# Kernel tuning notes

Measured on AMD Instinct MI355X. Metric: run time of the kernel, lower is better.

Reference implementation:

```python
import jax, jax.numpy as jnp
import numpy as np
from jax import lax

B, S, H = 32, 512, 128
NEG_INF = -1e30  # matches util.masked_softmax's large negative fill


def setup_inputs() -> dict:
    key = jax.random.key(0)
    ks = jax.random.split(key, 10)
    sc = 0.05
    vp = jax.random.normal(ks[0], (B, S, 2 * H), dtype=jnp.float32)
    # valid lengths in [S//2, S]; packed loop runs max(lengths) steps
    p_s_lengths = jax.random.randint(ks[1], (B,), S // 2, S + 1, dtype=jnp.int32)
    W_vP  = jax.random.normal(ks[2], (H, 2 * H), dtype=jnp.float32) * sc      # linear_vP.weight
    W_vPt = jax.random.normal(ks[3], (H, 2 * H), dtype=jnp.float32) * sc      # linear_vPt.weight
    w_vT  = jax.random.normal(ks[4], (H,), dtype=jnp.float32) * sc            # linear_vT.weight (1,H) -> vector
    W_g   = jax.random.normal(ks[5], (4 * H, 4 * H), dtype=jnp.float32) * sc  # g.weight
    W_ih  = jax.random.normal(ks[6], (3 * H, 4 * H), dtype=jnp.float32) * sc  # GRUCell.weight_ih
    W_hh  = jax.random.normal(ks[7], (3 * H, H), dtype=jnp.float32) * sc      # GRUCell.weight_hh
    b_ih  = jax.random.normal(ks[8], (3 * H,), dtype=jnp.float32) * sc
    b_hh  = jax.random.normal(ks[9], (3 * H,), dtype=jnp.float32) * sc
    return dict(vp=vp, p_s_lengths=p_s_lengths, W_vP=W_vP, W_vPt=W_vPt,
                w_vT=w_vT, W_g=W_g, W_ih=W_ih, W_hh=W_hh, b_ih=b_ih, b_hh=b_hh)


def _self_attn_rnn(vp, p_s_lengths, W_vP, W_vPt, w_vT, W_g, W_ih, W_hh, b_ih, b_hh):
    Bb, Ss, H2 = vp.shape
    Hh = H2 // 2
    s_idx = jnp.arange(Ss)

    # reverse_enc: reverse each sequence only over its valid prefix
    rev_idx = jnp.where(s_idx[None, :] < p_s_lengths[:, None],
                        p_s_lengths[:, None] - 1 - s_idx[None, :], s_idx[None, :])
    rev_vp = jnp.take_along_axis(vp, rev_idx[:, :, None], axis=1)

    bidir_vp = jnp.concatenate([vp, rev_vp], axis=0)       # (2B,S,2H) inputs per step
    vp2 = jnp.concatenate([vp, vp], axis=0)                 # (2B,S,2H) attention memory (forward order!)
    len2 = jnp.concatenate([p_s_lengths, p_s_lengths], 0)   # (2B,)

    keyp = jnp.einsum('bsd,hd->bsh', vp2, W_vP)             # precompute linear_vP(vp)
    seq_mask = s_idx[None, :] < len2[:, None]               # (2B,S)

    def step(h, inputs):
        x_t, active = inputs                                # (2B,2H), (2B,)
        q = x_t @ W_vPt.T                                   # (2B,H)
        logits = jnp.tanh(keyp + q[:, None, :]) @ w_vT      # (2B,S)
        a = jax.nn.softmax(jnp.where(seq_mask, logits, NEG_INF), axis=1)
        ct = jnp.einsum('bs,bsd->bd', a, vp2)               # (2B,2H)
        vpc = jnp.concatenate([x_t, ct], axis=-1)           # (2B,4H)
        gt = jax.nn.sigmoid(vpc @ W_g.T)
        xin = gt * vpc
        gi = xin @ W_ih.T + b_ih
        gh = h @ W_hh.T + b_hh
        ir, iz, inn = jnp.split(gi, 3, axis=-1)
        hr, hz, hn = jnp.split(gh, 3, axis=-1)
        r = jax.nn.sigmoid(ir + hr)
        z = jax.nn.sigmoid(iz + hz)
        n = jnp.tanh(inn + r * hn)
        h_new = (1.0 - z) * n + z * h
        # packed semantics: inactive (padded) slots keep zeros and never update again
        h_new = jnp.where(active[:, None], h_new, 0.0)
        return h_new, h_new

    xs = (jnp.swapaxes(bidir_vp, 0, 1), seq_mask.T)          # (S,2B,2H), (S,2B)
    h0 = jnp.zeros((2 * Bb, Hh), dtype=vp.dtype)
    _, hs = lax.scan(jax.checkpoint(step), h0, xs)           # hs: (S,2B,H)
    hp = jnp.swapaxes(hs, 0, 1)                              # (2B,S,H)
    # original concatenates fwd half and rev half on feature dim (rev half stays in reversed time order)
    return jnp.concatenate([hp[:Bb], hp[Bb:]], axis=-1)      # (B,S,2H)


def reference(vp, p_s_lengths, W_vP, W_vPt, w_vT, W_g, W_ih, W_hh, b_ih, b_hh):
    # dropout is identity at inference (training=False)
    return _self_attn_rnn(vp, p_s_lengths, W_vP, W_vPt, w_vT, W_g, W_ih, W_hh, b_ih, b_hh)
```

## Files before the change

kernel.cpp:

```cpp
#include <hip/hip_runtime.h>
#include <hip/hip_fp16.h>

#define BB 32
#define SS 512
#define HH 128
#define D2 256
#define D3 384
#define D4 512

#define OFF_TK  0
#define OFF_TQ  (OFF_TK + BB*SS*HH)
#define OFF_CT  (OFF_TQ + BB*SS*HH)
#define OFF_GI  (OFF_CT + BB*SS*D2)
#define OFF_F16 (OFF_GI + BB*SS*D3)
#define F16_WG  0
#define F16_WIH (F16_WG + D4*D4)
#define F16_W2  (F16_WIH + D3*D4)

typedef _Float16 f16x8 __attribute__((ext_vector_type(8)));
typedef _Float16 f16x4 __attribute__((ext_vector_type(4)));
typedef float    f32x4 __attribute__((ext_vector_type(4)));
typedef _Float16 h2_t  __attribute__((ext_vector_type(2)));

__device__ __forceinline__ float fast_tanh(float x) {
  float ax = fabsf(x);
  float e  = __expf(-2.0f * ax);
  float t  = __fdividef(1.0f - e, 1.0f + e);
  return x < 0.0f ? -t : t;
}
__device__ __forceinline__ float sigm(float x) {
  return __fdividef(1.0f, 1.0f + __expf(-x));
}

__global__ __launch_bounds__(256) void k0_prep(
    const float* __restrict__ Wg, const float* __restrict__ Wih,
    const float* __restrict__ Wvp, const float* __restrict__ Wvpt,
    float* __restrict__ ws) {
  int i = blockIdx.x * 256 + threadIdx.x;
  _Float16* f16b = (_Float16*)(ws + OFF_F16);
  if (i < D4 * D4) {
    f16b[F16_WG + i] = (_Float16)Wg[i];
  } else if (i < D4 * D4 + D3 * D4) {
    int j = i - D4 * D4;
    f16b[F16_WIH + j] = (_Float16)Wih[j];
  } else {
    int j = i - D4 * D4 - D3 * D4;
    f16b[F16_W2 + j] = (_Float16)(j < HH * D2 ? Wvp[j] : Wvpt[j - HH * D2]);
  }
}

__global__ __launch_bounds__(256, 2) void k1_keyq(const float* __restrict__ vp,
                                                  float* __restrict__ ws) {
  __shared__ __align__(16) _Float16 vpH[64 * 256];
  int tid = threadIdx.x;
  int rows0 = blockIdx.x * 64;

  #pragma unroll
  for (int i = 0; i < 8; ++i) {
    int u = tid + i * 256;
    int r = u >> 5, c8 = u & 31;
    const float* src = vp + (size_t)(rows0 + r) * D2 + c8 * 8;
    float4 a = *(const float4*)src;
    float4 b = *(const float4*)(src + 4);
    f16x8 h;
    h[0]=(_Float16)a.x; h[1]=(_Float16)a.y; h[2]=(_Float16)a.z; h[3]=(_Float16)a.w;
    h[4]=(_Float16)b.x; h[5]=(_Float16)b.y; h[6]=(_Float16)b.z; h[7]=(_Float16)b.w;
    *(f16x8*)(&vpH[r * 256 + (c8 ^ (r & 7)) * 8]) = h;
  }
  __syncthreads();

  const _Float16* W2 = (const _Float16*)(ws + OFF_F16) + F16_W2;
  int w = tid >> 6, l = tid & 63;
  int lr = l & 15, lk = (l >> 4) * 8;

  f32x4 acc[4][4];
  #pragma unroll
  for (int m = 0; m < 4; ++m)
    #pragma unroll
    for (int n = 0; n < 4; ++n) acc[m][n] = (f32x4){0.f, 0.f, 0.f, 0.f};

  for (int kc = 0; kc < 8; ++kc) {
    int k = kc * 32 + lk;
    f16x8 bf[4];
    #pragma unroll
    for (int n = 0; n < 4; ++n) {
      int r = n * 16 + lr;
      bf[n] = *(const f16x8*)(&vpH[r * 256 + (((k >> 3) ^ (r & 7))) * 8]);
    }
    #pragma unroll
    for (int m = 0; m < 4; ++m) {
      int c = w * 64 + m * 16 + lr;
      f16x8 af = *(const f16x8*)(W2 + (size_t)c * 256 + k);
      #pragma unroll
      for (int n = 0; n < 4; ++n)
        acc[m][n] = __builtin_amdgcn_mfma_f32_16x16x32_f16(af, bf[n], acc[m][n], 0, 0, 0);
    }
  }

  int b = rows0 >> 9;
  int s0 = rows0 & 511;
  float* ekT = ws + OFF_TK + (size_t)b * HH * SS;
  float* eqp = ws + OFF_TQ + (size_t)b * SS * HH;
  #pragma unroll
  for (int m = 0; m < 4; ++m) {
    int c0 = w * 64 + m * 16 + (l >> 4) * 4;
    #pragma unroll
    for (int n = 0; n < 4; ++n) {
      int s = s0 + n * 16 + lr;
      float v[4];
      #pragma unroll
      for (int j = 0; j < 4; ++j) {
        float z = fminf(fmaxf(2.0f * acc[m][n][j], -60.0f), 60.0f);
        v[j] = __expf(z);
      }
      if (c0 < HH) {
        #pragma unroll
        for (int j = 0; j < 4; ++j)
          ekT[(size_t)(c0 + j) * SS + s] = v[j];
      } else {
        float4 o; o.x = v[0]; o.y = v[1]; o.z = v[2]; o.w = v[3];
        *(float4*)(eqp + (size_t)s * HH + (c0 - HH)) = o;
      }
    }
  }
}

__global__ __launch_bounds__(256) void k2_attn(const float* __restrict__ vp,
                                               const int* __restrict__ lens,
                                               const float* __restrict__ wvt,
                                               float* __restrict__ ws) {
  int bid = blockIdx.x;
  int b  = (bid & 7) * 4 + ((bid >> 3) & 3);
  int t0 = (bid >> 5) * 16;
  int len = lens[b];
  if (t0 >= len) return;
  int nt = min(16, len - t0);

  __shared__ float L[16][SS];
  __shared__ float Eqs[16][HH];
  __shared__ float inv_sum[16];

  int tid = threadIdx.x;
  const float* EkT = ws + OFF_TK + (size_t)b * HH * SS;
  const float* Eq  = ws + OFF_TQ + (size_t)b * SS * HH;

  for (int idx = tid; idx < 16 * HH; idx += 256) {
    int i = idx >> 7, h = idx & 127;
    Eqs[i][h] = Eq[(size_t)(t0 + i) * HH + h];
  }
  __syncthreads();

  for (int sc = 0; sc < 2; ++sc) {
    int s = tid + sc * 256;
    if (s < len) {
      float acc[16] = {};
      for (int h4 = 0; h4 < 32; ++h4) {
        float k0 = EkT[(size_t)(h4 * 4 + 0) * SS + s];
        float k1 = EkT[(size_t)(h4 * 4 + 1) * SS + s];
        float k2v = EkT[(size_t)(h4 * 4 + 2) * SS + s];
        float k3 = EkT[(size_t)(h4 * 4 + 3) * SS + s];
        const float4 w4 = *(const float4*)(wvt + h4 * 4);
        #pragma unroll
        for (int t = 0; t < 16; ++t) {
          const float4 q4 = *(const float4*)(&Eqs[t][h4 * 4]);
          float r0 = __builtin_amdgcn_rcpf(fmaf(k0, q4.x, 1.0f));
          float r1 = __builtin_amdgcn_rcpf(fmaf(k1, q4.y, 1.0f));
          float r2 = __builtin_amdgcn_rcpf(fmaf(k2v, q4.z, 1.0f));
          float r3 = __builtin_amdgcn_rcpf(fmaf(k3, q4.w, 1.0f));
          float a = acc[t];
          a = fmaf(w4.x, r0, a);
          a = fmaf(w4.y, r1, a);
          a = fmaf(w4.z, r2, a);
          a = fmaf(w4.w, r3, a);
          acc[t] = a;
        }
      }
      #pragma unroll
      for (int t = 0; t < 16; ++t) L[t][s] = -2.0f * acc[t];
    }
  }
  __syncthreads();

  {
    int w = tid >> 6, lane = tid & 63;
    for (int ii = 0; ii < 4; ++ii) {
      int i = w + ii * 4;
      if (i < nt) {
        float m = -1e30f;
        for (int s = lane; s < len; s += 64) m = fmaxf(m, L[i][s]);
        #pragma unroll
        for (int off = 32; off > 0; off >>= 1) m = fmaxf(m, __shfl_xor(m, off));
        float sm = 0.0f;
        for (int s = lane; s < len; s += 64) {
          float e = __expf(L[i][s] - m);
          L[i][s] = e;
          sm += e;
        }
        #pragma unroll
        for (int off = 32; off > 0; off >>= 1) sm += __shfl_xor(sm, off);
        if (lane == 0) inv_sum[i] = __fdividef(1.0f, sm);
      }
    }
  }
  __syncthreads();

  int d4 = (tid & 63) * 4;
  int tg = tid >> 6;
  float4 acc4[4] = {};
  const float* vpb = vp + (size_t)b * SS * D2;
  int s = 0;
  for (; s + 4 <= len; s += 4) {
    #pragma unroll
    for (int u = 0; u < 4; ++u) {
      float4 v4 = *(const float4*)(vpb + (size_t)(s + u) * D2 + d4);
      #pragma unroll
      for (int j = 0; j < 4; ++j) {
        float p = L[tg * 4 + j][s + u];
        acc4[j].x = fmaf(p, v4.x, acc4[j].x);
        acc4[j].y = fmaf(p, v4.y, acc4[j].y);
        acc4[j].z = fmaf(p, v4.z, acc4[j].z);
        acc4[j].w = fmaf(p, v4.w, acc4[j].w);
      }
    }
  }
  for (; s < len; ++s) {
    float4 v4 = *(const float4*)(vpb + (size_t)s * D2 + d4);
    #pragma unroll
    for (int j = 0; j < 4; ++j) {
      float p = L[tg * 4 + j][s];
      acc4[j].x = fmaf(p, v4.x, acc4[j].x);
      acc4[j].y = fmaf(p, v4.y, acc4[j].y);
      acc4[j].z = fmaf(p, v4.z, acc4[j].z);
      acc4[j].w = fmaf(p, v4.w, acc4[j].w);
    }
  }
  float* ctg = ws + OFF_CT + ((size_t)b * SS + t0) * D2;
  #pragma unroll
  for (int j = 0; j < 4; ++j) {
    int t = tg * 4 + j;
    if (t < nt) {
      float is = inv_sum[t];
      float4 o;
      o.x = acc4[j].x * is; o.y = acc4[j].y * is;
      o.z = acc4[j].z * is; o.w = acc4[j].w * is;
      *(float4*)(ctg + (size_t)t * D2 + d4) = o;
    }
  }
}

__global__ __launch_bounds__(256, 2) void k3_gates(const float* __restrict__ vp,
                                                   const int* __restrict__ lens,
                                                   const float* __restrict__ bih,
                                                   float* __restrict__ ws) {
  int b = blockIdx.y;
  int len = lens[b];
  int t0 = blockIdx.x * 32;
  if (t0 >= len) return;

  __shared__ __align__(16) _Float16 vpcH[32 * 512];
  int tid = threadIdx.x;
  const float* ct = ws + OFF_CT;

  #pragma unroll
  for (int i = 0; i < 8; ++i) {
    int u = tid + i * 256;
    int r = u >> 6, c8 = u & 63;
    int c = c8 * 8;
    const float* src = (c < D2) ? (vp + ((size_t)b * SS + t0 + r) * D2 + c)
                                : (ct + ((size_t)b * SS + t0 + r) * D2 + (c - D2));
    float4 a = *(const float4*)src;
    float4 bb = *(const float4*)(src + 4);
    f16x8 h;
    h[0]=(_Float16)a.x;  h[1]=(_Float16)a.y;  h[2]=(_Float16)a.z;  h[3]=(_Float16)a.w;
    h[4]=(_Float16)bb.x; h[5]=(_Float16)bb.y; h[6]=(_Float16)bb.z; h[7]=(_Float16)bb.w;
    *(f16x8*)(&vpcH[r * 512 + (c8 ^ (r & 7)) * 8]) = h;
  }
  __syncthreads();

  const _Float16* WgH  = (const _Float16*)(ws + OFF_F16) + F16_WG;
  const _Float16* WihH = (const _Float16*)(ws + OFF_F16) + F16_WIH;
  int w = tid >> 6, l = tid & 63;
  int lr = l & 15, lk = (l >> 4) * 8;

  f32x4 acc[8][2];
  #pragma unroll
  for (int m = 0; m < 8; ++m) { acc[m][0] = (f32x4){0.f,0.f,0.f,0.f}; acc[m][1] = (f32x4){0.f,0.f,0.f,0.f}; }

  for (int kc = 0; kc < 16; ++kc) {
    int k = kc * 32 + lk;
    f16x8 bf[2];
    #pragma unroll
    for (int n = 0; n < 2; ++n) {
      int r = n * 16 + lr;
      bf[n] = *(const f16x8*)(&vpcH[r * 512 + (((k >> 3) ^ (r & 7))) * 8]);
    }
    #pragma unroll
    for (int m = 0; m < 8; ++m) {
      int c = w * 128 + m * 16 + lr;
      f16x8 af = *(const f16x8*)(WgH + (size_t)c * 512 + k);
      acc[m][0] = __builtin_amdgcn_mfma_f32_16x16x32_f16(af, bf[0], acc[m][0], 0, 0, 0);
      acc[m][1] = __builtin_amdgcn_mfma_f32_16x16x32_f16(af, bf[1], acc[m][1], 0, 0, 0);
    }
  }

  f16x4 xq[8][2];
  #pragma unroll
  for (int m = 0; m < 8; ++m) {
    int c0 = w * 128 + m * 16 + (l >> 4) * 4;
    #pragma unroll
    for (int n = 0; n < 2; ++n) {
      int r = n * 16 + lr;
      int ea = r * 512 + (((c0 >> 3) ^ (r & 7))) * 8 + (c0 & 7);
      f16x4 vq = *(const f16x4*)(&vpcH[ea]);
      f16x4 xo;
      #pragma unroll
      for (int j = 0; j < 4; ++j)
        xo[j] = (_Float16)(sigm(acc[m][n][j]) * (float)vq[j]);
      xq[m][n] = xo;
    }
  }
  __syncthreads();
  #pragma unroll
  for (int m = 0; m < 8; ++m) {
    int c0 = w * 128 + m * 16 + (l >> 4) * 4;
    #pragma unroll
    for (int n = 0; n < 2; ++n) {
      int r = n * 16 + lr;
      int ea = r * 512 + (((c0 >> 3) ^ (r & 7))) * 8 + (c0 & 7);
      *(f16x4*)(&vpcH[ea]) = xq[m][n];
    }
  }
  __syncthreads();

  f32x4 gacc[6][2];
  #pragma unroll
  for (int m = 0; m < 6; ++m) { gacc[m][0] = (f32x4){0.f,0.f,0.f,0.f}; gacc[m][1] = (f32x4){0.f,0.f,0.f,0.f}; }

  for (int kc = 0; kc < 16; ++kc) {
    int k = kc * 32 + lk;
    f16x8 bf[2];
    #pragma unroll
    for (int n = 0; n < 2; ++n) {
      int r = n * 16 + lr;
      bf[n] = *(const f16x8*)(&vpcH[r * 512 + (((k >> 3) ^ (r & 7))) * 8]);
    }
    #pragma unroll
    for (int m = 0; m < 6; ++m) {
      int c = w * 96 + m * 16 + lr;
      f16x8 af = *(const f16x8*)(WihH + (size_t)c * 512 + k);
      gacc[m][0] = __builtin_amdgcn_mfma_f32_16x16x32_f16(af, bf[0], gacc[m][0], 0, 0, 0);
      gacc[m][1] = __builtin_amdgcn_mfma_f32_16x16x32_f16(af, bf[1], gacc[m][1], 0, 0, 0);
    }
  }

  float* gig = ws + OFF_GI;
  #pragma unroll
  for (int m = 0; m < 6; ++m) {
    int c0 = w * 96 + m * 16 + (l >> 4) * 4;
    float4 bq = *(const float4*)(bih + c0);
    #pragma unroll
    for (int n = 0; n < 2; ++n) {
      int r = n * 16 + lr;
      float4 o;
      o.x = gacc[m][n][0] + bq.x;
      o.y = gacc[m][n][1] + bq.y;
      o.z = gacc[m][n][2] + bq.z;
      o.w = gacc[m][n][3] + bq.w;
      *(float4*)(gig + ((size_t)b * SS + t0 + r) * D3 + c0) = o;
    }
  }
}

__global__ __launch_bounds__(384) void k4_scan(const float* __restrict__ whh,
                                               const float* __restrict__ bhh,
                                               const int* __restrict__ lens,
                                               const float* __restrict__ ws,
                                               float* __restrict__ out) {
  int bid = blockIdx.x;
  int xcd = bid & 7, dir = (bid >> 3) & 1, q = bid >> 4;
  int b = xcd * 4 + q;
  int len = lens[b];
  int tid = threadIdx.x;
  const float* gi = ws + OFF_GI + (size_t)b * SS * D3;

  h2_t wr[64];
  {
    const float* wrow = whh + (size_t)tid * HH;
    #pragma unroll
    for (int k = 0; k < 64; ++k)
      wr[k] = h2_t{(_Float16)wrow[2 * k], (_Float16)wrow[2 * k + 1]};
  }
  float bh = bhh[tid];

  __shared__ __align__(16) _Float16 hbuf[128];
  __shared__ float gsum[D3];
  if (tid < 128) hbuf[tid] = (_Float16)0.0f;
  float h_own = 0.0f;

  float* outb = out + (size_t)b * SS * D2 + dir * HH;

#define K4_BAR() do {                                                          \
    asm volatile("s_waitcnt lgkmcnt(0)" ::: "memory");                         \
    __builtin_amdgcn_s_barrier();                                              \
    __builtin_amdgcn_sched_barrier(0);                                         \
  } while (0)

#define K4_PF(gx0, gx1, gx2, tnext) do {                                       \
    if (tid < 128) {                                                           \
      int tp = (tnext) < len ? (tnext) : (len - 1);                            \
      int tgp = dir ? (len - 1 - tp) : tp;                                     \
      const float* gp = gi + (size_t)tgp * D3;                                 \
      gx0 = gp[tid]; gx1 = gp[tid + 128]; gx2 = gp[tid + 256];                 \
    }                                                                          \
  } while (0)

#define K4_DOT() do {                                                          \
    const f16x8* hb8 = (const f16x8*)hbuf;                                     \
    float c0 = 0.f, c1 = 0.f, c2 = 0.f, c3 = 0.f;                              \
    _Pragma("unroll")                                                          \
    for (int k8 = 0; k8 < 16; ++k8) {                                          \
      f16x8 hv = hb8[k8];                                                      \
      c0 = __builtin_amdgcn_fdot2(__builtin_shufflevector(hv, hv, 0, 1),       \
                                  wr[4 * k8 + 0], c0, false);                  \
      c1 = __builtin_amdgcn_fdot2(__builtin_shufflevector(hv, hv, 2, 3),       \
                                  wr[4 * k8 + 1], c1, false);                  \
      c2 = __builtin_amdgcn_fdot2(__builtin_shufflevector(hv, hv, 4, 5),       \
                                  wr[4 * k8 + 2], c2, false);                  \
      c3 = __builtin_amdgcn_fdot2(__builtin_shufflevector(hv, hv, 6, 7),       \
                                  wr[4 * k8 + 3], c3, false);                  \
    }                                                                          \
    gsum[tid] = ((c0 + c1) + (c2 + c3)) + bh;                                  \
  } while (0)

#define K4_COMBINE(gx0, gx1, gx2, tstep) do {                                  \
    if (tid < 128) {                                                           \
      float r = sigm((gx0) + gsum[tid]);                                       \
      float z = sigm((gx1) + gsum[tid + 128]);                                 \
      float n = fast_tanh(fmaf(r, gsum[tid + 256], (gx2)));                    \
      float hn = (1.0f - z) * n + z * h_own;                                   \
      h_own = hn;                                                              \
      outb[(size_t)(tstep) * D2 + tid] = hn;                                   \
      hbuf[tid] = (_Float16)hn;                                                \
    }                                                                          \
  } while (0)

#define K4_STEP(gx0, gx1, gx2, tstep) do {                                     \
    K4_DOT();                                                                  \
    K4_BAR();                                                                  \
    K4_COMBINE(gx0, gx1, gx2, (tstep));                                        \
    K4_PF(gx0, gx1, gx2, (tstep) + 4);                                         \
    K4_BAR();                                                                  \
  } while (0)

  float gA0 = 0.f, gA1 = 0.f, gA2 = 0.f;
  float gB0 = 0.f, gB1 = 0.f, gB2 = 0.f;
  float gC0 = 0.f, gC1 = 0.f, gC2 = 0.f;
  float gD0 = 0.f, gD1 = 0.f, gD2 = 0.f;
  K4_PF(gA0, gA1, gA2, 0);
  K4_PF(gB0, gB1, gB2, 1);
  K4_PF(gC0, gC1, gC2, 2);
  K4_PF(gD0, gD1, gD2, 3);
  K4_BAR();

  int t = 0;
  while (t + 3 < len) {
    K4_STEP(gA0, gA1, gA2, t);
    K4_STEP(gB0, gB1, gB2, t + 1);
    K4_STEP(gC0, gC1, gC2, t + 2);
    K4_STEP(gD0, gD1, gD2, t + 3);
    t += 4;
  }
  if (t < len)     K4_STEP(gA0, gA1, gA2, t);
  if (t + 1 < len) K4_STEP(gB0, gB1, gB2, t + 1);
  if (t + 2 < len) K4_STEP(gC0, gC1, gC2, t + 2);

#undef K4_STEP
#undef K4_COMBINE
#undef K4_DOT
#undef K4_PF
#undef K4_BAR
}

extern "C" void kernel_launch(void* const* d_in, const int* in_sizes, int n_in,
                              void* d_out, int out_size, void* d_ws, size_t ws_size,
                              hipStream_t stream) {
  const float* vp   = (const float*)d_in[0];
  const int*   lens = (const int*)d_in[1];
  const float* Wvp  = (const float*)d_in[2];
  const float* Wvpt = (const float*)d_in[3];
  const float* wvt  = (const float*)d_in[4];
  const float* Wg   = (const float*)d_in[5];
  const float* Wih  = (const float*)d_in[6];
  const float* Whh  = (const float*)d_in[7];
  const float* bih  = (const float*)d_in[8];
  const float* bhh  = (const float*)d_in[9];
  float* out = (float*)d_out;
  float* ws  = (float*)d_ws;

  hipMemsetAsync(d_out, 0, (size_t)out_size * sizeof(float), stream);

  k0_prep<<<2048, 256, 0, stream>>>(Wg, Wih, Wvp, Wvpt, ws);
  k1_keyq<<<BB * SS / 64, 256, 0, stream>>>(vp, ws);
  k2_attn<<<1024, 256, 0, stream>>>(vp, lens, wvt, ws);
  k3_gates<<<dim3(SS / 32, BB), 256, 0, stream>>>(vp, lens, bih, ws);
  k4_scan<<<64, 384, 0, stream>>>(Whh, bhh, lens, ws, out);
}
```

Baseline: 573.2 us.

## Collapse GRU scan to 128 threads computing all three gates per thread

The recurrent scan kernel now launches 128 threads instead of 384, and each thread holds all three W_hh gate rows in registers. The hidden-gate sums no longer round-trip through shared memory, and one of the two barriers per timestep is removed. Hidden state is double-buffered in LDS so the write for the next step cannot race with reads of the current one. Each step does three times more dot work per thread and uses many more registers, in exchange for shorter serial latency per step.

Measured after the change: 606.3 us. 5.8% more time.

```diff
diff --git a/kernel.cpp b/kernel.cpp
--- a/kernel.cpp
+++ b/kernel.cpp
@@ -371,11 +371,11 @@
   }
 }
 
-__global__ __launch_bounds__(384) void k4_scan(const float* __restrict__ whh,
-                                               const float* __restrict__ bhh,
-                                               const int* __restrict__ lens,
-                                               const float* __restrict__ ws,
-                                               float* __restrict__ out) {
+__global__ __launch_bounds__(128, 1) void k4_scan(const float* __restrict__ whh,
+                                                  const float* __restrict__ bhh,
+                                                  const int* __restrict__ lens,
+                                                  const float* __restrict__ ws,
+                                                  float* __restrict__ out) {
   int bid = blockIdx.x;
   int xcd = bid & 7, dir = (bid >> 3) & 1, q = bid >> 4;
   int b = xcd * 4 + q;
@@ -383,18 +383,22 @@
   int tid = threadIdx.x;
   const float* gi = ws + OFF_GI + (size_t)b * SS * D3;
 
-  h2_t wr[64];
+  h2_t w0[64], w1[64], w2[64];
   {
-    const float* wrow = whh + (size_t)tid * HH;
-    #pragma unroll
-    for (int k = 0; k < 64; ++k)
-      wr[k] = h2_t{(_Float16)wrow[2 * k], (_Float16)wrow[2 * k + 1]};
-  }
-  float bh = bhh[tid];
-
-  __shared__ __align__(16) _Float16 hbuf[128];
-  __shared__ float gsum[D3];
-  if (tid < 128) hbuf[tid] = (_Float16)0.0f;
+    const float* r0 = whh + (size_t)tid * HH;
+    const float* r1 = whh + (size_t)(tid + 128) * HH;
+    const float* r2 = whh + (size_t)(tid + 256) * HH;
+    #pragma unroll
+    for (int k = 0; k < 64; ++k) {
+      w0[k] = h2_t{(_Float16)r0[2 * k], (_Float16)r0[2 * k + 1]};
+      w1[k] = h2_t{(_Float16)r1[2 * k], (_Float16)r1[2 * k + 1]};
+      w2[k] = h2_t{(_Float16)r2[2 * k], (_Float16)r2[2 * k + 1]};
+    }
+  }
+  float bh0 = bhh[tid], bh1 = bhh[tid + 128], bh2 = bhh[tid + 256];
+
+  __shared__ __align__(16) _Float16 hbuf[2][128];
+  hbuf[0][tid] = (_Float16)0.0f;
   float h_own = 0.0f;
 
   float* outb = out + (size_t)b * SS * D2 + dir * HH;
@@ -406,56 +410,52 @@
   } while (0)
 
 #define K4_PF(gx0, gx1, gx2, tnext) do {                                       \
-    if (tid < 128) {                                                           \
-      int tp = (tnext) < len ? (tnext) : (len - 1);                            \
-      int tgp = dir ? (len - 1 - tp) : tp;                                     \
-      const float* gp = gi + (size_t)tgp * D3;                                 \
-      gx0 = gp[tid]; gx1 = gp[tid + 128]; gx2 = gp[tid + 256];                 \
-    }                                                                          \
+    int tp = (tnext) < len ? (tnext) : (len - 1);                              \
+    int tgp = dir ? (len - 1 - tp) : tp;                                       \
+    const float* gp = gi + (size_t)tgp * D3;                                   \
+    gx0 = gp[tid]; gx1 = gp[tid + 128]; gx2 = gp[tid + 256];                   \
   } while (0)
 
-#define K4_DOT() do {                                                          \
-    const f16x8* hb8 = (const f16x8*)hbuf;                                     \
-    float c0 = 0.f, c1 = 0.f, c2 = 0.f, c3 = 0.f;                              \
+#define K4_STEP(gx0, gx1, gx2, tstep, PB) do {                                 \
+    const f16x8* hb8 = (const f16x8*)hbuf[PB];                                 \
+    float a00 = 0.f, a01 = 0.f, a02 = 0.f, a03 = 0.f;                          \
+    float a10 = 0.f, a11 = 0.f, a12 = 0.f, a13 = 0.f;                          \
+    float a20 = 0.f, a21 = 0.f, a22 = 0.f, a23 = 0.f;                          \
     _Pragma("unroll")                                                          \
     for (int k8 = 0; k8 < 16; ++k8) {                                          \
       f16x8 hv = hb8[k8];                                                      \
-      c0 = __builtin_amdgcn_fdot2(__builtin_shufflevector(hv, hv, 0, 1),       \
-                                  wr[4 * k8 + 0], c0, false);                  \
-      c1 = __builtin_amdgcn_fdot2(__builtin_shufflevector(hv, hv, 2, 3),       \
-                                  wr[4 * k8 + 1], c1, false);                  \
-      c2 = __builtin_amdgcn_fdot2(__builtin_shufflevector(hv, hv, 4, 5),       \
-                                  wr[4 * k8 + 2], c2, false);                  \
-      c3 = __builtin_amdgcn_fdot2(__builtin_shufflevector(hv, hv, 6, 7),       \
-                                  wr[4 * k8 + 3], c3, false);                  \
+      h2_t p0 = __builtin_shufflevector(hv, hv, 0, 1);                         \
+      h2_t p1 = __builtin_shufflevector(hv, hv, 2, 3);                         \
+      h2_t p2 = __builtin_shufflevector(hv, hv, 4, 5);                         \
+      h2_t p3 = __builtin_shufflevector(hv, hv, 6, 7);                         \
+      a00 = __builtin_amdgcn_fdot2(p0, w0[4 * k8 + 0], a00, false);            \
+      a01 = __builtin_amdgcn_fdot2(p1, w0[4 * k8 + 1], a01, false);            \
+      a02 = __builtin_amdgcn_fdot2(p2, w0[4 * k8 + 2], a02, false);            \
+      a03 = __builtin_amdgcn_fdot2(p3, w0[4 * k8 + 3], a03, false);            \
+      a10 = __builtin_amdgcn_fdot2(p0, w1[4 * k8 + 0], a10, false);            \
+      a11 = __builtin_amdgcn_fdot2(p1, w1[4 * k8 + 1], a11, false);            \
+      a12 = __builtin_amdgcn_fdot2(p2, w1[4 * k8 + 2], a12, false);            \
+      a13 = __builtin_amdgcn_fdot2(p3, w1[4 * k8 + 3], a13, false);            \
+      a20 = __builtin_amdgcn_fdot2(p0, w2[4 * k8 + 0], a20, false);            \
+      a21 = __builtin_amdgcn_fdot2(p1, w2[4 * k8 + 1], a21, false);            \
+      a22 = __builtin_amdgcn_fdot2(p2, w2[4 * k8 + 2], a22, false);            \
+      a23 = __builtin_amdgcn_fdot2(p3, w2[4 * k8 + 3], a23, false);            \
     }                                                                          \
-    gsum[tid] = ((c0 + c1) + (c2 + c3)) + bh;                                  \
-  } while (0)
-
-#define K4_COMBINE(gx0, gx1, gx2, tstep) do {                                  \
-    if (tid < 128) {                                                           \
-      float r = sigm((gx0) + gsum[tid]);                                       \
-      float z = sigm((gx1) + gsum[tid + 128]);                                 \
-      float n = fast_tanh(fmaf(r, gsum[tid + 256], (gx2)));                    \
-      float hn = (1.0f - z) * n + z * h_own;                                   \
-      h_own = hn;                                                              \
-      outb[(size_t)(tstep) * D2 + tid] = hn;                                   \
-      hbuf[tid] = (_Float16)hn;                                                \
-    }                                                                          \
-  } while (0)
-
-#define K4_STEP(gx0, gx1, gx2, tstep) do {                                     \
-    K4_DOT();                                                                  \
-    K4_BAR();                                                                  \
-    K4_COMBINE(gx0, gx1, gx2, (tstep));                                        \
+    float gh0 = ((a00 + a01) + (a02 + a03)) + bh0;                             \
+    float gh1 = ((a10 + a11) + (a12 + a13)) + bh1;                             \
+    float gh2 = ((a20 + a21) + (a22 + a23)) + bh2;                             \
+    float r = sigm((gx0) + gh0);                                               \
+    float z = sigm((gx1) + gh1);                                               \
+    float n = fast_tanh(fmaf(r, gh2, (gx2)));                                  \
+    float hn = (1.0f - z) * n + z * h_own;                                     \
+    h_own = hn;                                                                \
+    outb[(size_t)(tstep) * D2 + tid] = hn;                                     \
+    hbuf[(PB) ^ 1][tid] = (_Float16)hn;                                        \
     K4_PF(gx0, gx1, gx2, (tstep) + 4);                                         \
     K4_BAR();                                                                  \
   } while (0)
 
-  float gA0 = 0.f, gA1 = 0.f, gA2 = 0.f;
-  float gB0 = 0.f, gB1 = 0.f, gB2 = 0.f;
-  float gC0 = 0.f, gC1 = 0.f, gC2 = 0.f;
-  float gD0 = 0.f, gD1 = 0.f, gD2 = 0.f;
+  float gA0, gA1, gA2, gB0, gB1, gB2, gC0, gC1, gC2, gD0, gD1, gD2;
   K4_PF(gA0, gA1, gA2, 0);
   K4_PF(gB0, gB1, gB2, 1);
   K4_PF(gC0, gC1, gC2, 2);
@@ -464,19 +464,17 @@
 
   int t = 0;
   while (t + 3 < len) {
-    K4_STEP(gA0, gA1, gA2, t);
-    K4_STEP(gB0, gB1, gB2, t + 1);
-    K4_STEP(gC0, gC1, gC2, t + 2);
-    K4_STEP(gD0, gD1, gD2, t + 3);
+    K4_STEP(gA0, gA1, gA2, t,     0);
+    K4_STEP(gB0, gB1, gB2, t + 1, 1);
+    K4_STEP(gC0, gC1, gC2, t + 2, 0);
+    K4_STEP(gD0, gD1, gD2, t + 3, 1);
     t += 4;
   }
-  if (t < len)     K4_STEP(gA0, gA1, gA2, t);
-  if (t + 1 < len) K4_STEP(gB0, gB1, gB2, t + 1);
-  if (t + 2 < len) K4_STEP(gC0, gC1, gC2, t + 2);
+  if (t < len)     K4_STEP(gA0, gA1, gA2, t,     0);
+  if (t + 1 < len) K4_STEP(gB0, gB1, gB2, t + 1, 1);
+  if (t + 2 < len) K4_STEP(gC0, gC1, gC2, t + 2, 0);
 
 #undef K4_STEP
-#undef K4_COMBINE
-#undef K4_DOT
 #undef K4_PF
 #undef K4_BAR
 }
@@ -503,5 +501,5 @@
   k1_keyq<<<BB * SS / 64, 256, 0, stream>>>(vp, ws);
   k2_attn<<<1024, 256, 0, stream>>>(vp, lens, wvt, ws);
   k3_gates<<<dim3(SS / 32, BB), 256, 0, stream>>>(vp, lens, bih, ws);
-  k4_scan<<<64, 384, 0, stream>>>(Whh, bhh, lens, ws, out);
-}
+  k4_scan<<<64, 128, 0, stream>>>(Whh, bhh, lens, ws, out);
+}
```
